# Performance work log

Hardware: AMD Instinct MI355X
Metric: run time of the kernel (lower is better)

The kernel has to match this reference:

```python
import jax, jax.numpy as jnp
import numpy as np

SPIKE_THRESHOLD = 0.01


def setup_inputs() -> dict:
    key = jax.random.key(0)
    k_x, k_w1, k_w2 = jax.random.split(key, 3)
    B, T, S, D, F = 4, 16, 512, 512, 2048
    x = jax.random.normal(k_x, (B, T, S, D), dtype=jnp.float32)
    # FFN parameters (the wrapped `model`): Linear(D,F) -> ReLU -> Linear(F,D)
    w1 = jax.random.normal(k_w1, (D, F), dtype=jnp.float32) * (1.0 / np.sqrt(D))
    b1 = jnp.zeros((F,), dtype=jnp.float32)
    w2 = jax.random.normal(k_w2, (F, D), dtype=jnp.float32) * (1.0 / np.sqrt(F))
    b2 = jnp.zeros((D,), dtype=jnp.float32)
    return {"x": x, "w1": w1, "b1": b1, "w2": w2, "b2": b2}


def reference(x, w1, b1, w2, b2):
    # x: [B, T, S, D]. Event-driven: rows with any |x| > threshold are
    # processed by the model; inactive rows produce zeros.
    spike_mask = jnp.any(jnp.abs(x) > SPIKE_THRESHOLD, axis=-1)  # [B, T, S]
    h = jax.nn.relu(jnp.einsum("btsd,df->btsf", x, w1) + b1)     # [B, T, S, F]
    y = jnp.einsum("btsf,fd->btsd", h, w2) + b2                   # [B, T, S, D]
    return jnp.where(spike_mask[..., None], y, jnp.zeros((), dtype=y.dtype))
```

## Files before the change

kernel.cpp:

```cpp
#include <hip/hip_runtime.h>
#include <hip/hip_bf16.h>

typedef __attribute__((ext_vector_type(8))) short bf16x8;
typedef __attribute__((ext_vector_type(16))) float f32x16;
typedef __attribute__((ext_vector_type(4))) unsigned u32x4;

#define TH 0.01f
#define MFMA32(a, b, c) __builtin_amdgcn_mfma_f32_32x32x16_bf16(a, b, c, 0, 0, 0)

constexpr int D = 512, F = 2048, BM = 128, NC = 64;

constexpr int W1A_O = 0;
constexpr int W1B_O = 32768;
constexpr int W2A_O = 65536;
constexpr int W2B_O = 98304;
constexpr int H2_0  = 131072;
constexpr int H2_1  = 139264;
constexpr int HP_O  = 147456;
constexpr int B1_O  = 155648;
constexpr int LDS_TOTAL = 163840;

static __device__ __forceinline__ short f2bf(float f) {
  union { float f; unsigned u; } v; v.f = f;
  unsigned r = v.u + 0x7FFFu + ((v.u >> 16) & 1u);
  return (short)(r >> 16);
}

static __device__ __forceinline__ void gl16(const void* g, char* l) {
  __builtin_amdgcn_global_load_lds(
      (const __attribute__((address_space(1))) unsigned*)g,
      (__attribute__((address_space(3))) unsigned*)l, 16, 0, 0);
}

__global__ void prep_weights(const float* __restrict__ w1, const float* __restrict__ w2,
                             short* __restrict__ w1s, short* __restrict__ w2s) {
  int G = blockIdx.x * 256 + threadIdx.x;
  if (G < 131072) {
    int c = G >> 11, g = G & 2047;
    int ks = g >> 6, lane = g & 63, l31 = lane & 31, l5 = lane >> 5;
    bf16x8 v;
#pragma unroll
    for (int j = 0; j < 8; ++j)
      v[j] = f2bf(w1[(size_t)(ks * 16 + l5 * 8 + j) * F + c * 32 + l31]);
    *(bf16x8*)(w1s + (size_t)G * 8) = v;
  } else {
    int H = G - 131072;
    int c = H >> 11, g = H & 2047;
    int ks = g >> 10, cf = (g >> 6) & 15, lane = g & 63, l31 = lane & 31, l5 = lane >> 5;
    bf16x8 v;
#pragma unroll
    for (int j = 0; j < 8; ++j)
      v[j] = f2bf(w2[(size_t)(c * 32 + ks * 16 + l5 * 8 + j) * D + cf * 32 + l31]);
    *(bf16x8*)(w2s + (size_t)H * 8) = v;
  }
}

#define ISSUE4(loff, gptr)                                                      \
  do {                                                                          \
    _Pragma("unroll") for (int _t = 0; _t < 4; ++_t)                            \
        gl16((const char*)(gptr) + (size_t)(_t * 512 + tid) * 16,               \
             smem + (loff) + (_t * 512 + tid) * 16);                            \
  } while (0)

__global__ __launch_bounds__(512, 2)
void ffn_fused(const float* __restrict__ x,
               const float* __restrict__ b1,
               const float* __restrict__ b2,
               const char* __restrict__ w1g,
               const char* __restrict__ w2g,
               float* __restrict__ out) {
  extern __shared__ char smem[];
  const int tid = threadIdx.x;
  const int lane = tid & 63, wid = tid >> 6;
  const int l31 = lane & 31, l5 = lane >> 5;
  const int row0 = blockIdx.x * BM;

  const int p  = wid & 3,  kh = wid >> 2;
  const int cq = wid & 3,  rh = wid >> 2;
  unsigned* tmpspk = (unsigned*)(smem + H2_0);

  if (tid < 4) tmpspk[tid] = 0u;
  ISSUE4(W1A_O, w1g);
  *(float4*)((float*)(smem + B1_O) + tid * 4) = *(const float4*)&b1[tid * 4];

  bf16x8 xr[16];
  for (int r = 0; r < 4; ++r) {
    {
      const float* xg = x + (size_t)(row0 + r * 32) * D;
      float* xs = (float*)(smem + W2A_O);
#pragma unroll
      for (int it = 0; it < 8; ++it) {
        int idx = it * 512 + tid;
        int rl = idx >> 7, col = (idx & 127) * 4;
        float4 v = *(const float4*)(xg + rl * 512 + col);
        *(float4*)(xs + rl * 512 + (col ^ ((rl & 7) << 2))) = v;
      }
    }
    asm volatile("s_waitcnt vmcnt(0) lgkmcnt(0)" ::: "memory");
    __builtin_amdgcn_s_barrier();
    if (p == r) {
      const float* xs = (const float*)(smem + W2A_O);
      bool rowany = false;
#pragma unroll
      for (int s = 0; s < 16; ++s) {
        int base = kh * 256 + s * 16 + l5 * 8;
        int c0 = base ^ ((l31 & 7) << 2);
        int c1 = (base + 4) ^ ((l31 & 7) << 2);
        float4 a4 = *(const float4*)(xs + l31 * 512 + c0);
        float4 b4 = *(const float4*)(xs + l31 * 512 + c1);
        rowany = rowany | (fabsf(a4.x) > TH) | (fabsf(a4.y) > TH) |
                 (fabsf(a4.z) > TH) | (fabsf(a4.w) > TH) | (fabsf(b4.x) > TH) |
                 (fabsf(b4.y) > TH) | (fabsf(b4.z) > TH) | (fabsf(b4.w) > TH);
        bf16x8 t;
        t[0] = f2bf(a4.x); t[1] = f2bf(a4.y); t[2] = f2bf(a4.z); t[3] = f2bf(a4.w);
        t[4] = f2bf(b4.x); t[5] = f2bf(b4.y); t[6] = f2bf(b4.z); t[7] = f2bf(b4.w);
        xr[s] = t;
      }
      unsigned long long bl = __ballot(rowany);
      if (lane == 0) atomicOr(&tmpspk[r], (unsigned)bl | (unsigned)(bl >> 32));
    }
    asm volatile("s_waitcnt lgkmcnt(0)" ::: "memory");
    __builtin_amdgcn_s_barrier();
  }
  const unsigned smv0 = tmpspk[rh * 2 + 0];
  const unsigned smv1 = tmpspk[rh * 2 + 1];
  asm volatile("s_waitcnt vmcnt(0) lgkmcnt(0)" ::: "memory");
  __builtin_amdgcn_s_barrier();

  ISSUE4(W1B_O, w1g + 32768);
  ISSUE4(W2A_O, w2g);

  f32x16 oacc[8];
#pragma unroll
  for (int n = 0; n < 8; ++n)
#pragma unroll
    for (int j = 0; j < 16; ++j) oacc[n][j] = 0.f;

  const float* b1s = (const float*)(smem + B1_O);

#pragma unroll 1
  for (int i = 0; i < NC; ++i) {
    const int sl = i & 1;
    f32x16 hacc;

    if (i < NC - 1) asm volatile("s_waitcnt vmcnt(8)" ::: "memory");
    else            asm volatile("s_waitcnt vmcnt(4)" ::: "memory");

    __builtin_amdgcn_s_setprio(1);
    if (i > 0) {
      const int js = (i - 1) & 1;
      const char* h2r  = smem + (js ? H2_1 : H2_0);
      const char* w2rd = smem + (js ? W2B_O : W2A_O);
#pragma unroll
      for (int ks = 0; ks < 2; ++ks) {
        bf16x8 hA0 = *(const bf16x8*)(h2r + ((2 * ks + l5) * 128 + rh * 64 + l31) * 16);
        bf16x8 hA1 = *(const bf16x8*)(h2r + ((2 * ks + l5) * 128 + rh * 64 + 32 + l31) * 16);
#pragma unroll
        for (int n = 0; n < 4; ++n) {
          bf16x8 wf = *(const bf16x8*)(w2rd + ks * 16384 + (cq * 4 + n) * 1024 + lane * 16);
          oacc[n]     = MFMA32(hA0, wf, oacc[n]);
          oacc[4 + n] = MFMA32(hA1, wf, oacc[4 + n]);
        }
      }
    }
    {
      const char* w1slot = smem + (sl ? W1B_O : W1A_O);
#pragma unroll
      for (int j = 0; j < 16; ++j) hacc[j] = 0.f;
#pragma unroll
      for (int s = 0; s < 16; ++s) {
        bf16x8 wf = *(const bf16x8*)(w1slot + (kh * 16 + s) * 1024 + lane * 16);
        hacc = MFMA32(wf, xr[s], hacc);
      }
    }
    __builtin_amdgcn_s_setprio(0);
    if (kh) {
      u32x4 pk0, pk1;
#pragma unroll
      for (int t = 0; t < 4; ++t) {
        pk0[t] = (unsigned)(unsigned short)f2bf(hacc[2 * t]) |
                 ((unsigned)(unsigned short)f2bf(hacc[2 * t + 1]) << 16);
        pk1[t] = (unsigned)(unsigned short)f2bf(hacc[8 + 2 * t]) |
                 ((unsigned)(unsigned short)f2bf(hacc[8 + 2 * t + 1]) << 16);
      }
      *(u32x4*)(smem + HP_O + p * 2048 + lane * 32) = pk0;
      *(u32x4*)(smem + HP_O + p * 2048 + lane * 32 + 16) = pk1;
    }
    asm volatile("s_waitcnt lgkmcnt(0)" ::: "memory");
    __builtin_amdgcn_s_barrier();

    if (!kh) {
      const char* hp = smem + HP_O + p * 2048;
      u32x4 q0 = *(const u32x4*)(hp + lane * 32);
      u32x4 q1 = *(const u32x4*)(hp + lane * 32 + 16);
#pragma unroll
      for (int t = 0; t < 4; ++t) {
        hacc[2 * t]     += __uint_as_float(q0[t] << 16);
        hacc[2 * t + 1] += __uint_as_float(q0[t] & 0xffff0000u);
        hacc[8 + 2 * t]     += __uint_as_float(q1[t] << 16);
        hacc[8 + 2 * t + 1] += __uint_as_float(q1[t] & 0xffff0000u);
      }
      char* h2w = smem + (sl ? H2_1 : H2_0);
#pragma unroll
      for (int q = 0; q < 4; ++q) {
        float4 bv = *(const float4*)&b1s[i * 32 + q * 8 + l5 * 4];
        short4 pk;
        pk.x = f2bf(fmaxf(hacc[4 * q + 0] + bv.x, 0.f));
        pk.y = f2bf(fmaxf(hacc[4 * q + 1] + bv.y, 0.f));
        pk.z = f2bf(fmaxf(hacc[4 * q + 2] + bv.z, 0.f));
        pk.w = f2bf(fmaxf(hacc[4 * q + 3] + bv.w, 0.f));
        *(short4*)(h2w + q * 2048 + (p * 32 + l31) * 16 + l5 * 8) = pk;
      }
    }
    if (i + 2 < NC) ISSUE4(sl ? W1B_O : W1A_O, w1g + (size_t)(i + 2) * 32768);
    if (i + 1 < NC) ISSUE4(((i + 1) & 1) ? W2B_O : W2A_O,
                           w2g + (size_t)(i + 1) * 32768);
    asm volatile("s_waitcnt lgkmcnt(0)" ::: "memory");
    __builtin_amdgcn_s_barrier();
  }

  asm volatile("s_waitcnt vmcnt(0)" ::: "memory");
  {
    const char* h2r  = smem + H2_1;
    const char* w2rd = smem + W2B_O;
    __builtin_amdgcn_s_setprio(1);
#pragma unroll
    for (int ks = 0; ks < 2; ++ks) {
      bf16x8 hA0 = *(const bf16x8*)(h2r + ((2 * ks + l5) * 128 + rh * 64 + l31) * 16);
      bf16x8 hA1 = *(const bf16x8*)(h2r + ((2 * ks + l5) * 128 + rh * 64 + 32 + l31) * 16);
#pragma unroll
      for (int n = 0; n < 4; ++n) {
        bf16x8 wf = *(const bf16x8*)(w2rd + ks * 16384 + (cq * 4 + n) * 1024 + lane * 16);
        oacc[n]     = MFMA32(hA0, wf, oacc[n]);
        oacc[4 + n] = MFMA32(hA1, wf, oacc[4 + n]);
      }
    }
    __builtin_amdgcn_s_setprio(0);
  }
#pragma unroll
  for (int rfi = 0; rfi < 2; ++rfi) {
    unsigned m = rfi ? smv1 : smv0;
#pragma unroll
    for (int n = 0; n < 4; ++n) {
      int dcol = cq * 128 + n * 32 + l31;
      float bias = b2[dcol];
      f32x16 acc = oacc[rfi * 4 + n];
#pragma unroll
      for (int r = 0; r < 16; ++r) {
        int rbit = (r & 3) + 8 * (r >> 2) + 4 * l5;
        int row = rh * 64 + rfi * 32 + rbit;
        float v = acc[r] + bias;
        out[(size_t)(row0 + row) * D + dcol] = ((m >> rbit) & 1u) ? v : 0.f;
      }
    }
  }
}

extern "C" void kernel_launch(void* const* d_in, const int* in_sizes, int n_in,
                              void* d_out, int out_size, void* d_ws, size_t ws_size,
                              hipStream_t stream) {
  const float* x  = (const float*)d_in[0];
  const float* w1 = (const float*)d_in[1];
  const float* b1 = (const float*)d_in[2];
  const float* w2 = (const float*)d_in[3];
  const float* b2 = (const float*)d_in[4];
  float* out = (float*)d_out;

  short* w1staged = (short*)d_ws;
  short* w2staged = w1staged + (size_t)D * F;

  prep_weights<<<1024, 256, 0, stream>>>(w1, w2, w1staged, w2staged);

  (void)hipFuncSetAttribute((const void*)ffn_fused,
                            hipFuncAttributeMaxDynamicSharedMemorySize, LDS_TOTAL);
  int M = out_size / D;
  ffn_fused<<<M / BM, 512, LDS_TOTAL, stream>>>(x, b1, b2, (const char*)w1staged,
                                                (const char*)w2staged, out);
}
```

Baseline: 164.6 us.

## Halve row tile to 64 with 256-thread blocks and single-buffered weights

```diff
diff --git a/kernel.cpp b/kernel.cpp
--- a/kernel.cpp
+++ b/kernel.cpp
@@ -8,17 +8,15 @@
 #define TH 0.01f
 #define MFMA32(a, b, c) __builtin_amdgcn_mfma_f32_32x32x16_bf16(a, b, c, 0, 0, 0)
 
-constexpr int D = 512, F = 2048, BM = 128, NC = 64;
-
-constexpr int W1A_O = 0;
-constexpr int W1B_O = 32768;
-constexpr int W2A_O = 65536;
-constexpr int W2B_O = 98304;
-constexpr int H2_0  = 131072;
-constexpr int H2_1  = 139264;
-constexpr int HP_O  = 147456;
-constexpr int B1_O  = 155648;
-constexpr int LDS_TOTAL = 163840;
+constexpr int D = 512, F = 2048, BM = 64, NC = 64;
+
+constexpr int W1_O  = 0;
+constexpr int W2_O  = 32768;
+constexpr int H2_0  = 65536;
+constexpr int H2_1  = 69632;
+constexpr int HP_O  = 73728;
+constexpr int SPK_O = 77824;
+constexpr int LDS_TOTAL = 77840;
 
 static __device__ __forceinline__ short f2bf(float f) {
   union { float f; unsigned u; } v; v.f = f;
@@ -55,14 +53,14 @@
   }
 }
 
-#define ISSUE4(loff, gptr)                                                      \
+#define ISSUE8(loff, gptr)                                                      \
   do {                                                                          \
-    _Pragma("unroll") for (int _t = 0; _t < 4; ++_t)                            \
-        gl16((const char*)(gptr) + (size_t)(_t * 512 + tid) * 16,               \
-             smem + (loff) + (_t * 512 + tid) * 16);                            \
+    _Pragma("unroll") for (int _t = 0; _t < 8; ++_t)                            \
+        gl16((const char*)(gptr) + (size_t)(_t * 256 + tid) * 16,               \
+             smem + (loff) + (_t * 256 + tid) * 16);                            \
   } while (0)
 
-__global__ __launch_bounds__(512, 2)
+__global__ __launch_bounds__(256, 2)
 void ffn_fused(const float* __restrict__ x,
                const float* __restrict__ b1,
                const float* __restrict__ b2,
@@ -75,22 +73,20 @@
   const int l31 = lane & 31, l5 = lane >> 5;
   const int row0 = blockIdx.x * BM;
 
-  const int p  = wid & 3,  kh = wid >> 2;
-  const int cq = wid & 3,  rh = wid >> 2;
-  unsigned* tmpspk = (unsigned*)(smem + H2_0);
-
-  if (tid < 4) tmpspk[tid] = 0u;
-  ISSUE4(W1A_O, w1g);
-  *(float4*)((float*)(smem + B1_O) + tid * 4) = *(const float4*)&b1[tid * 4];
+  const int p  = wid >> 1, kh = wid & 1;
+  const int cq = wid;
+  unsigned* spk = (unsigned*)(smem + SPK_O);
+
+  if (tid < 2) spk[tid] = 0u;
 
   bf16x8 xr[16];
-  for (int r = 0; r < 4; ++r) {
+  for (int r = 0; r < 2; ++r) {
     {
       const float* xg = x + (size_t)(row0 + r * 32) * D;
-      float* xs = (float*)(smem + W2A_O);
-#pragma unroll
-      for (int it = 0; it < 8; ++it) {
-        int idx = it * 512 + tid;
+      float* xs = (float*)(smem);
+#pragma unroll
+      for (int it = 0; it < 16; ++it) {
+        int idx = it * 256 + tid;
         int rl = idx >> 7, col = (idx & 127) * 4;
         float4 v = *(const float4*)(xg + rl * 512 + col);
         *(float4*)(xs + rl * 512 + (col ^ ((rl & 7) << 2))) = v;
@@ -99,7 +95,7 @@
     asm volatile("s_waitcnt vmcnt(0) lgkmcnt(0)" ::: "memory");
     __builtin_amdgcn_s_barrier();
     if (p == r) {
-      const float* xs = (const float*)(smem + W2A_O);
+      const float* xs = (const float*)(smem);
       bool rowany = false;
 #pragma unroll
       for (int s = 0; s < 16; ++s) {
@@ -117,44 +113,37 @@
         xr[s] = t;
       }
       unsigned long long bl = __ballot(rowany);
-      if (lane == 0) atomicOr(&tmpspk[r], (unsigned)bl | (unsigned)(bl >> 32));
+      if (lane == 0) atomicOr(&spk[r], (unsigned)bl | (unsigned)(bl >> 32));
     }
     asm volatile("s_waitcnt lgkmcnt(0)" ::: "memory");
     __builtin_amdgcn_s_barrier();
   }
-  const unsigned smv0 = tmpspk[rh * 2 + 0];
-  const unsigned smv1 = tmpspk[rh * 2 + 1];
+  const unsigned smv0 = spk[0];
+  const unsigned smv1 = spk[1];
+
+  ISSUE8(W1_O, w1g);
   asm volatile("s_waitcnt vmcnt(0) lgkmcnt(0)" ::: "memory");
   __builtin_amdgcn_s_barrier();
 
-  ISSUE4(W1B_O, w1g + 32768);
-  ISSUE4(W2A_O, w2g);
-
   f32x16 oacc[8];
 #pragma unroll
   for (int n = 0; n < 8; ++n)
 #pragma unroll
     for (int j = 0; j < 16; ++j) oacc[n][j] = 0.f;
-
-  const float* b1s = (const float*)(smem + B1_O);
 
 #pragma unroll 1
   for (int i = 0; i < NC; ++i) {
     const int sl = i & 1;
     f32x16 hacc;
 
-    if (i < NC - 1) asm volatile("s_waitcnt vmcnt(8)" ::: "memory");
-    else            asm volatile("s_waitcnt vmcnt(4)" ::: "memory");
-
     __builtin_amdgcn_s_setprio(1);
     if (i > 0) {
-      const int js = (i - 1) & 1;
-      const char* h2r  = smem + (js ? H2_1 : H2_0);
-      const char* w2rd = smem + (js ? W2B_O : W2A_O);
+      const char* h2r = smem + (((i - 1) & 1) ? H2_1 : H2_0);
+      const char* w2rd = smem + W2_O;
 #pragma unroll
       for (int ks = 0; ks < 2; ++ks) {
-        bf16x8 hA0 = *(const bf16x8*)(h2r + ((2 * ks + l5) * 128 + rh * 64 + l31) * 16);
-        bf16x8 hA1 = *(const bf16x8*)(h2r + ((2 * ks + l5) * 128 + rh * 64 + 32 + l31) * 16);
+        bf16x8 hA0 = *(const bf16x8*)(h2r + ((2 * ks + l5) * 64 + l31) * 16);
+        bf16x8 hA1 = *(const bf16x8*)(h2r + ((2 * ks + l5) * 64 + 32 + l31) * 16);
 #pragma unroll
         for (int n = 0; n < 4; ++n) {
           bf16x8 wf = *(const bf16x8*)(w2rd + ks * 16384 + (cq * 4 + n) * 1024 + lane * 16);
@@ -164,7 +153,7 @@
       }
     }
     {
-      const char* w1slot = smem + (sl ? W1B_O : W1A_O);
+      const char* w1slot = smem + W1_O;
 #pragma unroll
       for (int j = 0; j < 16; ++j) hacc[j] = 0.f;
 #pragma unroll
@@ -203,31 +192,32 @@
       char* h2w = smem + (sl ? H2_1 : H2_0);
 #pragma unroll
       for (int q = 0; q < 4; ++q) {
-        float4 bv = *(const float4*)&b1s[i * 32 + q * 8 + l5 * 4];
+        float4 bv = *(const float4*)&b1[i * 32 + q * 8 + l5 * 4];
         short4 pk;
         pk.x = f2bf(fmaxf(hacc[4 * q + 0] + bv.x, 0.f));
         pk.y = f2bf(fmaxf(hacc[4 * q + 1] + bv.y, 0.f));
         pk.z = f2bf(fmaxf(hacc[4 * q + 2] + bv.z, 0.f));
         pk.w = f2bf(fmaxf(hacc[4 * q + 3] + bv.w, 0.f));
-        *(short4*)(h2w + q * 2048 + (p * 32 + l31) * 16 + l5 * 8) = pk;
-      }
-    }
-    if (i + 2 < NC) ISSUE4(sl ? W1B_O : W1A_O, w1g + (size_t)(i + 2) * 32768);
-    if (i + 1 < NC) ISSUE4(((i + 1) & 1) ? W2B_O : W2A_O,
-                           w2g + (size_t)(i + 1) * 32768);
+        *(short4*)(h2w + q * 1024 + (p * 32 + l31) * 16 + l5 * 8) = pk;
+      }
+    }
     asm volatile("s_waitcnt lgkmcnt(0)" ::: "memory");
     __builtin_amdgcn_s_barrier();
-  }
-
-  asm volatile("s_waitcnt vmcnt(0)" ::: "memory");
+
+    if (i < NC - 1) ISSUE8(W1_O, w1g + (size_t)(i + 1) * 32768);
+    ISSUE8(W2_O, w2g + (size_t)i * 32768);
+    asm volatile("s_waitcnt vmcnt(0)" ::: "memory");
+    __builtin_amdgcn_s_barrier();
+  }
+
   {
-    const char* h2r  = smem + H2_1;
-    const char* w2rd = smem + W2B_O;
+    const char* h2r = smem + H2_1;
+    const char* w2rd = smem + W2_O;
     __builtin_amdgcn_s_setprio(1);
 #pragma unroll
     for (int ks = 0; ks < 2; ++ks) {
-      bf16x8 hA0 = *(const bf16x8*)(h2r + ((2 * ks + l5) * 128 + rh * 64 + l31) * 16);
-      bf16x8 hA1 = *(const bf16x8*)(h2r + ((2 * ks + l5) * 128 + rh * 64 + 32 + l31) * 16);
+      bf16x8 hA0 = *(const bf16x8*)(h2r + ((2 * ks + l5) * 64 + l31) * 16);
+      bf16x8 hA1 = *(const bf16x8*)(h2r + ((2 * ks + l5) * 64 + 32 + l31) * 16);
 #pragma unroll
       for (int n = 0; n < 4; ++n) {
         bf16x8 wf = *(const bf16x8*)(w2rd + ks * 16384 + (cq * 4 + n) * 1024 + lane * 16);
@@ -248,7 +238,7 @@
 #pragma unroll
       for (int r = 0; r < 16; ++r) {
         int rbit = (r & 3) + 8 * (r >> 2) + 4 * l5;
-        int row = rh * 64 + rfi * 32 + rbit;
+        int row = rfi * 32 + rbit;
         float v = acc[r] + bias;
         out[(size_t)(row0 + row) * D + dcol] = ((m >> rbit) & 1u) ? v : 0.f;
       }
@@ -274,6 +264,6 @@
   (void)hipFuncSetAttribute((const void*)ffn_fused,
                             hipFuncAttributeMaxDynamicSharedMemorySize, LDS_TOTAL);
   int M = out_size / D;
-  ffn_fused<<<M / BM, 512, LDS_TOTAL, stream>>>(x, b1, b2, (const char*)w1staged,
+  ffn_fused<<<M / BM, 256, LDS_TOTAL, stream>>>(x, b1, b2, (const char*)w1staged,
                                                 (const char*)w2staged, out);
 }
```

Result: slower. 217.7 us (+32.2%).

## Split fused FFN into two GEMM kernels with bf16 hidden buffer in workspace

Applied to the files above, without the earlier changes.

```diff
diff --git a/kernel.cpp b/kernel.cpp
--- a/kernel.cpp
+++ b/kernel.cpp
@@ -61,6 +61,187 @@
         gl16((const char*)(gptr) + (size_t)(_t * 512 + tid) * 16,               \
              smem + (loff) + (_t * 512 + tid) * 16);                            \
   } while (0)
+
+#define ISSUE1(loff, gptr)                                                      \
+  gl16((const char*)(gptr) + (size_t)tid * 16, smem + (loff) + (size_t)tid * 16)
+
+__global__ __launch_bounds__(512, 2)
+void g1_kernel(const float* __restrict__ x, const float* __restrict__ b1,
+               const char* __restrict__ w1g, char* __restrict__ hg,
+               unsigned* __restrict__ spikeg) {
+  extern __shared__ char smem[];
+  const int tid = threadIdx.x, lane = tid & 63, wid = tid >> 6;
+  const int l31 = lane & 31, l5 = lane >> 5;
+  const int rowblk = blockIdx.x >> 1, fh = blockIdx.x & 1;
+  const char* w1base = w1g + (size_t)(fh * 32) * 32768;
+
+  ISSUE4(0, w1base);
+  ISSUE4(32768, w1base + 32768);
+
+  bf16x8 xr[32];
+  float* xs = (float*)(smem + 65536);
+  for (int r = 0; r < 8; ++r) {
+    {
+      const float* xg = x + (size_t)(rowblk * 256 + r * 32) * D;
+#pragma unroll
+      for (int it = 0; it < 8; ++it) {
+        int idx = it * 512 + tid;
+        int rl = idx >> 7, col = (idx & 127) * 4;
+        float4 v = *(const float4*)(xg + rl * 512 + col);
+        *(float4*)(xs + rl * 512 + (col ^ ((rl & 7) << 2))) = v;
+      }
+    }
+    asm volatile("s_waitcnt vmcnt(0) lgkmcnt(0)" ::: "memory");
+    __builtin_amdgcn_s_barrier();
+    if (wid == r) {
+      bool any = false;
+#pragma unroll
+      for (int s = 0; s < 32; ++s) {
+        int base = s * 16 + l5 * 8;
+        int c0 = base ^ ((l31 & 7) << 2);
+        int c1 = (base + 4) ^ ((l31 & 7) << 2);
+        float4 a4 = *(const float4*)(xs + l31 * 512 + c0);
+        float4 b4 = *(const float4*)(xs + l31 * 512 + c1);
+        any = any | (fabsf(a4.x) > TH) | (fabsf(a4.y) > TH) | (fabsf(a4.z) > TH) |
+              (fabsf(a4.w) > TH) | (fabsf(b4.x) > TH) | (fabsf(b4.y) > TH) |
+              (fabsf(b4.z) > TH) | (fabsf(b4.w) > TH);
+        bf16x8 t;
+        t[0] = f2bf(a4.x); t[1] = f2bf(a4.y); t[2] = f2bf(a4.z); t[3] = f2bf(a4.w);
+        t[4] = f2bf(b4.x); t[5] = f2bf(b4.y); t[6] = f2bf(b4.z); t[7] = f2bf(b4.w);
+        xr[s] = t;
+      }
+      unsigned long long bl = __ballot(any);
+      if (lane == 0) spikeg[rowblk * 8 + r] = (unsigned)bl | (unsigned)(bl >> 32);
+    }
+    asm volatile("s_waitcnt lgkmcnt(0)" ::: "memory");
+    __builtin_amdgcn_s_barrier();
+  }
+
+  char* hbase = hg + (((size_t)(rowblk * 2 + (wid >> 2)) * 64 + fh * 32) * 8192) +
+                (wid & 3) * 2048 + l31 * 16 + l5 * 8;
+  const float* b1c = b1 + fh * 1024 + l5 * 4;
+
+#pragma unroll 1
+  for (int ch = 0; ch < 32; ++ch) {
+    asm volatile("s_waitcnt vmcnt(8)" ::: "memory");
+    __builtin_amdgcn_s_barrier();
+    const char* slot = smem + ((ch & 1) ? 32768 : 0);
+    float4 bv0 = *(const float4*)(b1c + ch * 32 + 0);
+    float4 bv1 = *(const float4*)(b1c + ch * 32 + 8);
+    float4 bv2 = *(const float4*)(b1c + ch * 32 + 16);
+    float4 bv3 = *(const float4*)(b1c + ch * 32 + 24);
+    f32x16 ha, hb;
+#pragma unroll
+    for (int j = 0; j < 16; ++j) { ha[j] = 0.f; hb[j] = 0.f; }
+    __builtin_amdgcn_s_setprio(1);
+#pragma unroll
+    for (int s = 0; s < 16; ++s) {
+      bf16x8 w0 = *(const bf16x8*)(slot + (2 * s) * 1024 + lane * 16);
+      bf16x8 w1f = *(const bf16x8*)(slot + (2 * s + 1) * 1024 + lane * 16);
+      ha = MFMA32(w0, xr[2 * s], ha);
+      hb = MFMA32(w1f, xr[2 * s + 1], hb);
+    }
+    __builtin_amdgcn_s_setprio(0);
+    char* hc = hbase + (size_t)ch * 8192;
+    {
+      short4 pk;
+      pk.x = f2bf(fmaxf(ha[0] + hb[0] + bv0.x, 0.f));
+      pk.y = f2bf(fmaxf(ha[1] + hb[1] + bv0.y, 0.f));
+      pk.z = f2bf(fmaxf(ha[2] + hb[2] + bv0.z, 0.f));
+      pk.w = f2bf(fmaxf(ha[3] + hb[3] + bv0.w, 0.f));
+      *(short4*)(hc + 0 * 512) = pk;
+      pk.x = f2bf(fmaxf(ha[4] + hb[4] + bv1.x, 0.f));
+      pk.y = f2bf(fmaxf(ha[5] + hb[5] + bv1.y, 0.f));
+      pk.z = f2bf(fmaxf(ha[6] + hb[6] + bv1.z, 0.f));
+      pk.w = f2bf(fmaxf(ha[7] + hb[7] + bv1.w, 0.f));
+      *(short4*)(hc + 1 * 512) = pk;
+      pk.x = f2bf(fmaxf(ha[8] + hb[8] + bv2.x, 0.f));
+      pk.y = f2bf(fmaxf(ha[9] + hb[9] + bv2.y, 0.f));
+      pk.z = f2bf(fmaxf(ha[10] + hb[10] + bv2.z, 0.f));
+      pk.w = f2bf(fmaxf(ha[11] + hb[11] + bv2.w, 0.f));
+      *(short4*)(hc + 2 * 512) = pk;
+      pk.x = f2bf(fmaxf(ha[12] + hb[12] + bv3.x, 0.f));
+      pk.y = f2bf(fmaxf(ha[13] + hb[13] + bv3.y, 0.f));
+      pk.z = f2bf(fmaxf(ha[14] + hb[14] + bv3.z, 0.f));
+      pk.w = f2bf(fmaxf(ha[15] + hb[15] + bv3.w, 0.f));
+      *(short4*)(hc + 3 * 512) = pk;
+    }
+    asm volatile("s_waitcnt lgkmcnt(0)" ::: "memory");
+    __builtin_amdgcn_s_barrier();
+    if (ch + 2 < 32) ISSUE4((ch & 1) ? 32768 : 0, w1base + (size_t)(ch + 2) * 32768);
+  }
+}
+
+__global__ __launch_bounds__(512, 2)
+void g2_kernel(const float* __restrict__ b2, const char* __restrict__ w2g,
+               const char* __restrict__ hg, const unsigned* __restrict__ spikeg,
+               float* __restrict__ out) {
+  extern __shared__ char smem[];
+  const int tid = threadIdx.x, lane = tid & 63, wid = tid >> 6;
+  const int l31 = lane & 31, l5 = lane >> 5;
+  const int cq = wid & 3, rh = wid >> 2;
+  const int mb = blockIdx.x;
+  const char* hgm = hg + (size_t)mb * 64 * 8192;
+
+  ISSUE1(65536, hgm);
+  ISSUE4(0, w2g);
+  ISSUE1(73728, hgm + 8192);
+  ISSUE4(32768, w2g + 32768);
+
+  f32x16 oacc[8];
+#pragma unroll
+  for (int n = 0; n < 8; ++n)
+#pragma unroll
+    for (int j = 0; j < 16; ++j) oacc[n][j] = 0.f;
+
+#pragma unroll 1
+  for (int kc = 0; kc < 64; ++kc) {
+    if (kc < 63) asm volatile("s_waitcnt vmcnt(5)" ::: "memory");
+    else         asm volatile("s_waitcnt vmcnt(0)" ::: "memory");
+    __builtin_amdgcn_s_barrier();
+    const char* hS  = smem + ((kc & 1) ? 73728 : 65536);
+    const char* w2S = smem + ((kc & 1) ? 32768 : 0);
+    __builtin_amdgcn_s_setprio(1);
+#pragma unroll
+    for (int ks = 0; ks < 2; ++ks) {
+      bf16x8 hA0 = *(const bf16x8*)(hS + (rh * 2 + 0) * 2048 + (2 * ks + l5) * 512 + l31 * 16);
+      bf16x8 hA1 = *(const bf16x8*)(hS + (rh * 2 + 1) * 2048 + (2 * ks + l5) * 512 + l31 * 16);
+#pragma unroll
+      for (int n = 0; n < 4; ++n) {
+        bf16x8 wf = *(const bf16x8*)(w2S + ks * 16384 + (cq * 4 + n) * 1024 + lane * 16);
+        oacc[n]     = MFMA32(hA0, wf, oacc[n]);
+        oacc[4 + n] = MFMA32(hA1, wf, oacc[4 + n]);
+      }
+    }
+    __builtin_amdgcn_s_setprio(0);
+    asm volatile("s_waitcnt lgkmcnt(0)" ::: "memory");
+    __builtin_amdgcn_s_barrier();
+    if (kc + 2 < 64) {
+      ISSUE1((kc & 1) ? 73728 : 65536, hgm + (size_t)(kc + 2) * 8192);
+      ISSUE4((kc & 1) ? 32768 : 0, w2g + (size_t)(kc + 2) * 32768);
+    }
+  }
+
+  unsigned mw0 = spikeg[mb * 4 + rh * 2 + 0];
+  unsigned mw1 = spikeg[mb * 4 + rh * 2 + 1];
+#pragma unroll
+  for (int rfi = 0; rfi < 2; ++rfi) {
+    unsigned m = rfi ? mw1 : mw0;
+#pragma unroll
+    for (int n = 0; n < 4; ++n) {
+      int dcol = cq * 128 + n * 32 + l31;
+      float bias = b2[dcol];
+      f32x16 acc = oacc[rfi * 4 + n];
+#pragma unroll
+      for (int r = 0; r < 16; ++r) {
+        int rbit = (r & 3) + 8 * (r >> 2) + 4 * l5;
+        int row = rh * 64 + rfi * 32 + rbit;
+        float v = acc[r] + bias;
+        out[(size_t)(mb * 128 + row) * D + dcol] = ((m >> rbit) & 1u) ? v : 0.f;
+      }
+    }
+  }
+}
 
 __global__ __launch_bounds__(512, 2)
 void ffn_fused(const float* __restrict__ x,
@@ -271,9 +452,26 @@
 
   prep_weights<<<1024, 256, 0, stream>>>(w1, w2, w1staged, w2staged);
 
-  (void)hipFuncSetAttribute((const void*)ffn_fused,
-                            hipFuncAttributeMaxDynamicSharedMemorySize, LDS_TOTAL);
   int M = out_size / D;
-  ffn_fused<<<M / BM, 512, LDS_TOTAL, stream>>>(x, b1, b2, (const char*)w1staged,
-                                                (const char*)w2staged, out);
-}
+  const size_t SPK_OFF = 4ull * 1024 * 1024;
+  const size_t H_OFF   = SPK_OFF + 65536;
+  const size_t NEED    = H_OFF + (size_t)M * F * 2;
+
+  if (ws_size >= NEED) {
+    unsigned* spikeg = (unsigned*)((char*)d_ws + SPK_OFF);
+    char* hg = (char*)d_ws + H_OFF;
+    (void)hipFuncSetAttribute((const void*)g1_kernel,
+                              hipFuncAttributeMaxDynamicSharedMemorySize, 131072);
+    (void)hipFuncSetAttribute((const void*)g2_kernel,
+                              hipFuncAttributeMaxDynamicSharedMemorySize, 81920);
+    g1_kernel<<<(M / 256) * 2, 512, 131072, stream>>>(
+        x, b1, (const char*)w1staged, hg, spikeg);
+    g2_kernel<<<M / 128, 512, 81920, stream>>>(
+        b2, (const char*)w2staged, hg, spikeg, out);
+  } else {
+    (void)hipFuncSetAttribute((const void*)ffn_fused,
+                              hipFuncAttributeMaxDynamicSharedMemorySize, LDS_TOTAL);
+    ffn_fused<<<M / BM, 512, LDS_TOTAL, stream>>>(
+        x, b1, b2, (const char*)w1staged, (const char*)w2staged, out);
+  }
+}
```

Result: slower. 316.5 us (+92.2%).
